# Kernel tuning notes

Measured on AMD Instinct MI355X. Metric: run time of the kernel, lower is better.

## Reference

```python
import jax, jax.numpy as jnp
import numpy as np

B, P, L, D, H = 32, 256, 64, 128, 8
DH = D // H
NP_, NL, E = B * P, B * L, B * P * L
LN_EPS = 1e-5


def setup_inputs() -> dict:
    key = jax.random.key(0)
    ks = jax.random.split(key, 32)
    def rn(i, shape, scale=0.05):
        return jax.random.normal(ks[i], shape, dtype=jnp.float32) * scale
    # uniform batch layout: graph b owns protein nodes [b*P,(b+1)*P) and ligand nodes [b*L,(b+1)*L)
    pe = (np.arange(B)[:, None] * P + np.repeat(np.arange(P), L)[None, :]).reshape(-1)
    le = (np.arange(B)[:, None] * L + np.tile(np.arange(L), P)[None, :]).reshape(-1)
    return {
        'h_protein': rn(0, (NP_, D), 1.0), 'h_ligand': rn(1, (NL, D), 1.0),
        'p_edge_idx': jnp.asarray(pe, jnp.int32), 'l_edge_idx': jnp.asarray(le, jnp.int32),
        'Wq_l': rn(2, (D, D)), 'Wk_p': rn(3, (D, D)), 'Wv_p': rn(4, (D, D)),
        'Wg_l': rn(5, (2 * D, D)), 'bg_l': jnp.zeros((D,), jnp.float32),
        'Wu_l': rn(6, (D, D)), 'bu_l': jnp.zeros((D,), jnp.float32),
        'Wq_p': rn(7, (D, D)), 'Wk_l': rn(8, (D, D)), 'Wv_l': rn(9, (D, D)),
        'Wg_p': rn(10, (2 * D, D)), 'bg_p': jnp.zeros((D,), jnp.float32),
        'Wu_p': rn(11, (D, D)), 'bu_p': jnp.zeros((D,), jnp.float32),
        'ln_p_g': jnp.ones((D,), jnp.float32), 'ln_p_b': jnp.zeros((D,), jnp.float32),
        'ln_l_g': jnp.ones((D,), jnp.float32), 'ln_l_b': jnp.zeros((D,), jnp.float32),
        'W1_p': rn(12, (D, 4 * D)), 'b1_p': jnp.zeros((4 * D,), jnp.float32),
        'W2_p': rn(13, (4 * D, D)), 'b2_p': jnp.zeros((D,), jnp.float32),
        'W1_l': rn(14, (D, 4 * D)), 'b1_l': jnp.zeros((4 * D,), jnp.float32),
        'W2_l': rn(15, (4 * D, D)), 'b2_l': jnp.zeros((D,), jnp.float32),
    }


def _layernorm(x, g, b):
    mu = jnp.mean(x, axis=-1, keepdims=True)
    var = jnp.mean(jnp.square(x - mu), axis=-1, keepdims=True)
    return (x - mu) * jax.lax.rsqrt(var + LN_EPS) * g + b


def _seg_softmax(scores, seg, n):  # scores [E,H], seg [E]
    m = jax.ops.segment_max(scores, seg, num_segments=n)
    e = jnp.exp(scores - m[seg])
    s = jax.ops.segment_sum(e, seg, num_segments=n)
    return e / s[seg]


def _side(hq, hkv, q_edge, kv_edge, nq, Wq, Wk, Wv, Wg, bg, Wu, bu):
    q = (hq @ Wq).reshape(-1, H, DH)
    k = (hkv @ Wk).reshape(-1, H, DH)
    v = (hkv @ Wv).reshape(-1, H, DH)
    scores = jnp.sum(q[q_edge] * k[kv_edge], axis=-1) / np.sqrt(DH)  # [E,H]
    att = _seg_softmax(scores, q_edge, nq)
    ctx = jax.ops.segment_sum(v[kv_edge] * att[:, :, None], q_edge, num_segments=nq)
    ctx = ctx.reshape(nq, D)
    gate = jax.nn.sigmoid(jnp.concatenate([hq, ctx], axis=1) @ Wg + bg)
    return hq + gate * (ctx @ Wu + bu)


def reference(h_protein, h_ligand, p_edge_idx, l_edge_idx,
              Wq_l, Wk_p, Wv_p, Wg_l, bg_l, Wu_l, bu_l,
              Wq_p, Wk_l, Wv_l, Wg_p, bg_p, Wu_p, bu_p,
              ln_p_g, ln_p_b, ln_l_g, ln_l_b,
              W1_p, b1_p, W2_p, b2_p, W1_l, b1_l, W2_l, b2_l):
    n_p, n_l = h_protein.shape[0], h_ligand.shape[0]
    # ligand attends to protein
    h_l_upd = _side(h_ligand, h_protein, l_edge_idx, p_edge_idx, n_l,
                    Wq_l, Wk_p, Wv_p, Wg_l, bg_l, Wu_l, bu_l)
    # protein attends to ligand
    h_p_upd = _side(h_protein, h_ligand, p_edge_idx, l_edge_idx, n_p,
                    Wq_p, Wk_l, Wv_l, Wg_p, bg_p, Wu_p, bu_p)
    # FFN blocks (dropout = identity in eval mode)
    hp = _layernorm(h_p_upd, ln_p_g, ln_p_b)
    protein_final = h_p_upd + jax.nn.relu(hp @ W1_p + b1_p) @ W2_p + b2_p
    hl = _layernorm(h_l_upd, ln_l_g, ln_l_b)
    ligand_final = h_l_upd + jax.nn.relu(hl @ W1_l + b1_l) @ W2_l + b2_l
    return (protein_final, ligand_final)
```

## Files before the change

kernel.cpp:

```cpp
#include <hip/hip_runtime.h>
#include <hip/hip_bf16.h>

typedef __bf16 bf16x8 __attribute__((ext_vector_type(8)));
typedef __bf16 bf16x4 __attribute__((ext_vector_type(4)));
typedef float  f32x4  __attribute__((ext_vector_type(4)));
typedef unsigned short u16;

#define NPROT 8192
#define NLIG  2048
#define DMODEL 128
#define NHEAD 8
#define NBATCH 32
#define PPB 256
#define LPB 64

__device__ __forceinline__ u16 f2bf(float f){
  union { float f; unsigned int u; } v; v.f = f;
  return (u16)((v.u + 0x7FFFu + ((v.u >> 16) & 1u)) >> 16);
}

__device__ __forceinline__ bf16x8 cvt8(const float* p){
  float4 a = *(const float4*)p, b = *(const float4*)(p + 4);
  bf16x8 r;
  r[0]=(__bf16)a.x; r[1]=(__bf16)a.y; r[2]=(__bf16)a.z; r[3]=(__bf16)a.w;
  r[4]=(__bf16)b.x; r[5]=(__bf16)b.y; r[6]=(__bf16)b.z; r[7]=(__bf16)b.w;
  return r;
}

struct QkvJob { const float* A; const float* Wsrc[3]; u16* outB; int blockStart; };
struct TJob { const float* src; u16* dst; int M, K, tilesX, blockStart; };
struct L1Args {
  QkvJob qjobs[2];
  int nQkv;
  int nprep;
  TJob pjobs[10];
};

__global__ __launch_bounds__(256) void l1_kernel(L1Args a){
  __shared__ u16 Wl[64][136];
  __shared__ u16 Al[64][136];
  __shared__ float tile[32][33];
  int bid = (int)blockIdx.x;
  int tid = (int)threadIdx.x;
  if (bid < a.nQkv){
    int j = (bid >= a.qjobs[1].blockStart) ? 1 : 0;
    const QkvJob jb = a.qjobs[j];
    int t = bid - jb.blockStart;
    int tn = t / 6, tm = t - tn * 6;
    {
      int midx = tm >> 1;
      int cb64 = (tm & 1) * 64;
      const float* Ws = jb.Wsrc[midx];
      int kr = tid >> 2;
      int cb = (tid & 3) * 16;
      #pragma unroll
      for (int p = 0; p < 2; ++p){
        int k = p * 64 + kr;
        const float* srcp = Ws + (size_t)k * 128 + cb64 + cb;
        float4 v0 = *(const float4*)srcp,     v1 = *(const float4*)(srcp + 4);
        float4 v2 = *(const float4*)(srcp+8), v3 = *(const float4*)(srcp + 12);
        float tmp[16] = {v0.x,v0.y,v0.z,v0.w, v1.x,v1.y,v1.z,v1.w,
                         v2.x,v2.y,v2.z,v2.w, v3.x,v3.y,v3.z,v3.w};
        #pragma unroll
        for (int i = 0; i < 16; ++i) Wl[cb + i][k] = f2bf(tmp[i]);
      }
    }
    {
      const float* Asrc = jb.A + (size_t)(tn * 64) * 128;
      #pragma unroll
      for (int p = 0; p < 8; ++p){
        int idx = p * 256 + tid;
        int r = idx >> 5, c4 = (idx & 31) * 4;
        float4 v = *(const float4*)(Asrc + (size_t)r * 128 + c4);
        Al[r][c4+0] = f2bf(v.x); Al[r][c4+1] = f2bf(v.y);
        Al[r][c4+2] = f2bf(v.z); Al[r][c4+3] = f2bf(v.w);
      }
    }
    __syncthreads();
    int w = tid >> 6, l = tid & 63;
    int rloc = (w >> 1) * 32;
    int cloc = (w & 1) * 32;
    int lr = l & 15, lk = (l >> 4) * 8;
    f32x4 a00 = {0.f,0.f,0.f,0.f}, a01 = a00, a10 = a00, a11 = a00;
    #pragma unroll
    for (int kk = 0; kk < 128; kk += 32){
      bf16x8 a0 = *(const bf16x8*)&Al[rloc + lr][kk + lk];
      bf16x8 a1 = *(const bf16x8*)&Al[rloc + 16 + lr][kk + lk];
      bf16x8 b0 = *(const bf16x8*)&Wl[cloc + lr][kk + lk];
      bf16x8 b1 = *(const bf16x8*)&Wl[cloc + 16 + lr][kk + lk];
      a00 = __builtin_amdgcn_mfma_f32_16x16x32_bf16(a0, b0, a00, 0, 0, 0);
      a01 = __builtin_amdgcn_mfma_f32_16x16x32_bf16(a0, b1, a01, 0, 0, 0);
      a10 = __builtin_amdgcn_mfma_f32_16x16x32_bf16(a1, b0, a10, 0, 0, 0);
      a11 = __builtin_amdgcn_mfma_f32_16x16x32_bf16(a1, b1, a11, 0, 0, 0);
    }
    int rbase = tn * 64 + rloc + ((l >> 4) << 2);
    f32x4 av[2][2] = {{a00, a01}, {a10, a11}};
    #pragma unroll
    for (int i = 0; i < 2; ++i)
      #pragma unroll
      for (int jj = 0; jj < 2; ++jj)
        #pragma unroll
        for (int e = 0; e < 4; ++e){
          int rr = rbase + i * 16 + e;
          int cc = tm * 64 + cloc + jj * 16 + lr;
          jb.outB[(size_t)rr * 384 + cc] = f2bf(av[i][jj][e]);
        }
  } else {
    int pb = bid - a.nQkv;
    int j = 0;
    while (j + 1 < a.nprep && pb >= a.pjobs[j + 1].blockStart) ++j;
    const TJob jb = a.pjobs[j];
    int t = pb - jb.blockStart;
    int tm = t % jb.tilesX, tk = t / jb.tilesX;
    int c = tid & 31, r0 = tid >> 5;
    #pragma unroll
    for (int p = 0; p < 4; ++p)
      tile[r0 + p * 8][c] = jb.src[(size_t)(tk * 32 + r0 + p * 8) * jb.M + tm * 32 + c];
    __syncthreads();
    {
      int c2 = tid >> 7;
      int lch = (tid >> 1) & 63;
      int eh = (tid & 1) * 4;
      int kl = (lch >> 4) * 8 + eh;
      int ml = c2 * 16 + (lch & 15);
      ushort4 o;
      o.x = f2bf(tile[kl + 0][ml]);
      o.y = f2bf(tile[kl + 1][ml]);
      o.z = f2bf(tile[kl + 2][ml]);
      o.w = f2bf(tile[kl + 3][ml]);
      size_t off = ((size_t)(tm * 2 + c2) * (jb.K >> 5) + tk) * 512 + lch * 8 + eh;
      *(ushort4*)&jb.dst[off] = o;
    }
  }
}

struct K2Args {
  const u16 *qkv_p, *qkv_l;
  const float *h_f[2];
  const u16 *WgT[2], *WgB[2], *WuT[2];
  const float *bg[2], *bu[2], *lng[2], *lnb[2];
  const u16 *W1T[2], *W2T[2];
  const float *b1[2], *b2[2];
  float* out[2];
};

struct K2B {
  float hu[32 * 132];
  union { float hstg[32 * 132]; u16 t[32 * 520]; } x;
};

__global__ __launch_bounds__(512) void k2_kernel(K2Args args){
  __shared__ __align__(16) union {
    struct { u16 vT[8 * 1152]; u16 P[8 * 2304]; } a;
    K2B b;
  } su;
  __shared__ __align__(16) u16 s_ctx[32 * 128];

  int bid = (int)blockIdx.x;
  int tid = (int)threadIdx.x;
  int w = tid >> 6, l = tid & 63, lr = l & 15, lg4 = l >> 4;
  int lk = lg4 * 8;

  int side, rowbase, batch, NC;
  if (bid < NLIG / 32){ side = 1; rowbase = bid * 32; batch = rowbase >> 6; NC = 4; }
  else { side = 0; rowbase = (bid - NLIG / 32) * 32; batch = rowbase >> 8; NC = 1; }

  const u16* qrow = (side == 0 ? args.qkv_p : args.qkv_l) + (size_t)rowbase * 384;
  const u16* orow = (side == 0 ? args.qkv_l : args.qkv_p)
                    + (size_t)(side == 0 ? batch * LPB : batch * PPB) * 384;

  bf16x8 zero8;
  #pragma unroll
  for (int i = 0; i < 8; ++i) zero8[i] = (__bf16)0.f;

  u16* vTw = su.a.vT + w * 1152;
  u16* Pw  = su.a.P  + w * 2304;
  int h = w;

  {
    bf16x8 qf[2];
    #pragma unroll
    for (int qt = 0; qt < 2; ++qt)
      qf[qt] = (l < 32) ? *(const bf16x8*)(qrow + (size_t)(qt * 16 + lr) * 384 + h * 16 + lk) : zero8;
    f32x4 Ot[2]; float mv[2], ls[2];
    #pragma unroll
    for (int qt = 0; qt < 2; ++qt){ Ot[qt] = (f32x4){0.f,0.f,0.f,0.f}; mv[qt] = -1e30f; ls[qt] = 0.f; }
    for (int c = 0; c < NC; ++c){
      {
        const u16* vs = orow + (size_t)(c * 64 + l) * 384 + 256 + h * 16;
        bf16x8 v0 = *(const bf16x8*)vs;
        bf16x8 v1 = *(const bf16x8*)(vs + 8);
        #pragma unroll
        for (int i = 0; i < 8; ++i){
          vTw[i * 72 + l]       = ((const u16*)&v0)[i];
          vTw[(i + 8) * 72 + l] = ((const u16*)&v1)[i];
        }
      }
      bf16x8 kf[4];
      #pragma unroll
      for (int kt = 0; kt < 4; ++kt)
        kf[kt] = (l < 32) ? *(const bf16x8*)(orow + (size_t)(c * 64 + kt * 16 + lr) * 384 + 128 + h * 16 + lk) : zero8;
      f32x4 sa[4][2];
      #pragma unroll
      for (int kt = 0; kt < 4; ++kt)
        #pragma unroll
        for (int qt = 0; qt < 2; ++qt)
          sa[kt][qt] = __builtin_amdgcn_mfma_f32_16x16x32_bf16(kf[kt], qf[qt], (f32x4){0.f,0.f,0.f,0.f}, 0, 0, 0);
      #pragma unroll
      for (int qt = 0; qt < 2; ++qt){
        float cm = -1e30f;
        #pragma unroll
        for (int kt = 0; kt < 4; ++kt)
          #pragma unroll
          for (int e = 0; e < 4; ++e) cm = fmaxf(cm, sa[kt][qt][e]);
        cm = fmaxf(cm, __shfl_xor(cm, 16)); cm = fmaxf(cm, __shfl_xor(cm, 32));
        float mn = fmaxf(mv[qt], cm);
        float resc = __expf((mv[qt] - mn) * 0.25f);
        mv[qt] = mn;
        float cs = 0.f;
        #pragma unroll
        for (int kt = 0; kt < 4; ++kt){
          bf16x4 pk;
          #pragma unroll
          for (int e = 0; e < 4; ++e){
            float p = __expf((sa[kt][qt][e] - mn) * 0.25f);
            cs += p; pk[e] = (__bf16)p;
          }
          *(bf16x4*)&Pw[(size_t)(qt * 16 + lr) * 72 + kt * 16 + lg4 * 4] = pk;
        }
        cs += __shfl_xor(cs, 16); cs += __shfl_xor(cs, 32);
        ls[qt] = ls[qt] * resc + cs;
        Ot[qt] = Ot[qt] * resc;
      }
      #pragma unroll
      for (int ks = 0; ks < 2; ++ks){
        bf16x8 va = *(const bf16x8*)&vTw[(size_t)lr * 72 + ks * 32 + lg4 * 8];
        #pragma unroll
        for (int qt = 0; qt < 2; ++qt){
          bf16x8 pb = *(const bf16x8*)&Pw[(size_t)(qt * 16 + lr) * 72 + ks * 32 + lg4 * 8];
          Ot[qt] = __builtin_amdgcn_mfma_f32_16x16x32_bf16(va, pb, Ot[qt], 0, 0, 0);
        }
      }
    }
    #pragma unroll
    for (int qt = 0; qt < 2; ++qt){
      float inv = 1.f / ls[qt];
      int q = qt * 16 + lr;
      int dbase = h * 16 + lg4 * 4;
      bf16x4 ov;
      #pragma unroll
      for (int e = 0; e < 4; ++e) ov[e] = (__bf16)(Ot[qt][e] * inv);
      *(bf16x4*)&s_ctx[(size_t)q * 128 + (dbase ^ ((q & 7) << 3))] = ov;
    }
  }
  __syncthreads();

  {
    const float* hsrc = args.h_f[side] + (size_t)rowbase * 128;
    #pragma unroll
    for (int p = 0; p < 2; ++p){
      int idx = p * 512 + tid;
      int r = idx >> 5, c4 = (idx & 31) * 4;
      *(float4*)&su.b.x.hstg[(size_t)r * 132 + c4] = *(const float4*)(hsrc + (size_t)r * 128 + c4);
    }
  }
  __syncthreads();

  {
    bf16x8 wg[4], wc[4], wu[4];
    {
      const u16* bgp = args.WgT[side] + (size_t)(w * 4) * 512 + l * 8;
      const u16* bcp = args.WgB[side] + (size_t)(w * 4) * 512 + l * 8;
      const u16* bup = args.WuT[side] + (size_t)(w * 4) * 512 + l * 8;
      #pragma unroll
      for (int kb = 0; kb < 4; ++kb) wg[kb] = *(const bf16x8*)(bgp + kb * 512);
      #pragma unroll
      for (int kb = 0; kb < 4; ++kb) wc[kb] = *(const bf16x8*)(bcp + kb * 512);
      #pragma unroll
      for (int kb = 0; kb < 4; ++kb) wu[kb] = *(const bf16x8*)(bup + kb * 512);
    }
    f32x4 g0 = {0.f,0.f,0.f,0.f}, g1 = g0, u0 = g0, u1 = g0;
    const float* hst = su.b.x.hstg;
    int swa = (lr & 7) << 3;
    #pragma unroll
    for (int kb = 0; kb < 4; ++kb){
      int kk = kb * 32;
      bf16x8 ah0 = cvt8(hst + (size_t)lr * 132 + kk);
      bf16x8 ah1 = cvt8(hst + (size_t)(16 + lr) * 132 + kk);
      bf16x8 ac0 = *(const bf16x8*)&s_ctx[(size_t)lr * 128 + ((kk + lk) ^ swa)];
      bf16x8 ac1 = *(const bf16x8*)&s_ctx[(size_t)(16 + lr) * 128 + ((kk + lk) ^ swa)];
      g0 = __builtin_amdgcn_mfma_f32_16x16x32_bf16(ah0, wg[kb], g0, 0, 0, 0);
      g1 = __builtin_amdgcn_mfma_f32_16x16x32_bf16(ah1, wg[kb], g1, 0, 0, 0);
      g0 = __builtin_amdgcn_mfma_f32_16x16x32_bf16(ac0, wc[kb], g0, 0, 0, 0);
      g1 = __builtin_amdgcn_mfma_f32_16x16x32_bf16(ac1, wc[kb], g1, 0, 0, 0);
      u0 = __builtin_amdgcn_mfma_f32_16x16x32_bf16(ac0, wu[kb], u0, 0, 0, 0);
      u1 = __builtin_amdgcn_mfma_f32_16x16x32_bf16(ac1, wu[kb], u1, 0, 0, 0);
    }
    int col = w * 16 + lr;
    float bgc = args.bg[side][col];
    float buc = args.bu[side][col];
    #pragma unroll
    for (int i = 0; i < 2; ++i){
      f32x4 gv4 = i ? g1 : g0;
      f32x4 uv4 = i ? u1 : u0;
      #pragma unroll
      for (int e = 0; e < 4; ++e){
        int row = i * 16 + lg4 * 4 + e;
        float gv = gv4[e] + bgc;
        float uv = uv4[e] + buc;
        float hv = hst[(size_t)row * 132 + col];
        float sg = 1.f / (1.f + __expf(-gv));
        su.b.hu[(size_t)row * 132 + col] = hv + sg * uv;
      }
    }
  }
  __syncthreads();

  {
    int r = tid >> 4;
    int sub = tid & 15;
    float x[8];
    #pragma unroll
    for (int i = 0; i < 2; ++i){
      float4 v4 = *(const float4*)&su.b.hu[(size_t)r * 132 + sub * 8 + i * 4];
      x[i*4+0] = v4.x; x[i*4+1] = v4.y; x[i*4+2] = v4.z; x[i*4+3] = v4.w;
    }
    float s = 0.f;
    #pragma unroll
    for (int i = 0; i < 8; ++i) s += x[i];
    s += __shfl_xor(s, 1); s += __shfl_xor(s, 2); s += __shfl_xor(s, 4); s += __shfl_xor(s, 8);
    float mu = s * (1.f / 128.f);
    float vv = 0.f;
    #pragma unroll
    for (int i = 0; i < 8; ++i){ float d = x[i] - mu; vv += d * d; }
    vv += __shfl_xor(vv, 1); vv += __shfl_xor(vv, 2); vv += __shfl_xor(vv, 4); vv += __shfl_xor(vv, 8);
    float rs = rsqrtf(vv * (1.f / 128.f) + 1e-5f);
    const float* lg2 = args.lng[side];
    const float* lb = args.lnb[side];
    int sw = (r & 7) << 3;
    #pragma unroll
    for (int i = 0; i < 8; ++i){
      int col = sub * 8 + i;
      s_ctx[(size_t)r * 128 + (col ^ sw)] = f2bf((x[i] - mu) * rs * lg2[col] + lb[col]);
    }
  }
  __syncthreads();

  {
    bf16x8 w1f[16];
    {
      const u16* b1p = args.W1T[side] + (size_t)(w * 16) * 512 + l * 8;
      #pragma unroll
      for (int q = 0; q < 16; ++q) w1f[q] = *(const bf16x8*)(b1p + q * 512);
    }
    f32x4 acc[2][4];
    #pragma unroll
    for (int i = 0; i < 2; ++i)
      #pragma unroll
      for (int jj = 0; jj < 4; ++jj) acc[i][jj] = (f32x4){0.f,0.f,0.f,0.f};
    int sw0 = (lr & 7) << 3;
    #pragma unroll
    for (int kb = 0; kb < 4; ++kb){
      int kk = kb * 32;
      bf16x8 a0 = *(const bf16x8*)&s_ctx[(size_t)lr * 128 + ((kk + lk) ^ sw0)];
      bf16x8 a1 = *(const bf16x8*)&s_ctx[(size_t)(16 + lr) * 128 + ((kk + lk) ^ sw0)];
      #pragma unroll
      for (int jj = 0; jj < 4; ++jj){
        acc[0][jj] = __builtin_amdgcn_mfma_f32_16x16x32_bf16(a0, w1f[jj * 4 + kb], acc[0][jj], 0, 0, 0);
        acc[1][jj] = __builtin_amdgcn_mfma_f32_16x16x32_bf16(a1, w1f[jj * 4 + kb], acc[1][jj], 0, 0, 0);
      }
    }
    const float* b1v = args.b1[side];
    u16* t_flat = su.b.x.t;
    #pragma unroll
    for (int i = 0; i < 2; ++i)
      #pragma unroll
      for (int jj = 0; jj < 4; ++jj)
        #pragma unroll
        for (int e = 0; e < 4; ++e){
          int row = i * 16 + lg4 * 4 + e;
          int col = w * 64 + jj * 16 + lr;
          float v = fmaxf(acc[i][jj][e] + b1v[col], 0.f);
          t_flat[(size_t)row * 520 + (col ^ ((row & 7) << 3))] = f2bf(v);
        }
  }
  __syncthreads();

  {
    bf16x8 w2f[16];
    {
      const u16* b2p = args.W2T[side] + (size_t)(w * 16) * 512 + l * 8;
      #pragma unroll
      for (int q = 0; q < 16; ++q) w2f[q] = *(const bf16x8*)(b2p + q * 512);
    }
    f32x4 o[2][2];
    #pragma unroll
    for (int i = 0; i < 2; ++i)
      #pragma unroll
      for (int p = 0; p < 2; ++p) o[i][p] = (f32x4){0.f,0.f,0.f,0.f};
    const u16* t_flat = su.b.x.t;
    int sw0 = (lr & 7) << 3;
    #pragma unroll
    for (int kb = 0; kb < 16; kb += 2){
      int kk = kb * 32;
      bf16x8 a0e = *(const bf16x8*)&t_flat[(size_t)lr * 520 + ((kk + lk) ^ sw0)];
      bf16x8 a1e = *(const bf16x8*)&t_flat[(size_t)(16 + lr) * 520 + ((kk + lk) ^ sw0)];
      bf16x8 a0o = *(const bf16x8*)&t_flat[(size_t)lr * 520 + ((kk + 32 + lk) ^ sw0)];
      bf16x8 a1o = *(const bf16x8*)&t_flat[(size_t)(16 + lr) * 520 + ((kk + 32 + lk) ^ sw0)];
      o[0][0] = __builtin_amdgcn_mfma_f32_16x16x32_bf16(a0e, w2f[kb],     o[0][0], 0, 0, 0);
      o[1][0] = __builtin_amdgcn_mfma_f32_16x16x32_bf16(a1e, w2f[kb],     o[1][0], 0, 0, 0);
      o[0][1] = __builtin_amdgcn_mfma_f32_16x16x32_bf16(a0o, w2f[kb + 1], o[0][1], 0, 0, 0);
      o[1][1] = __builtin_amdgcn_mfma_f32_16x16x32_bf16(a1o, w2f[kb + 1], o[1][1], 0, 0, 0);
    }
    const float* b2v = args.b2[side];
    float* outp = args.out[side];
    int col = w * 16 + lr;
    float b2c = b2v[col];
    #pragma unroll
    for (int i = 0; i < 2; ++i){
      #pragma unroll
      for (int e = 0; e < 4; ++e){
        int row = i * 16 + lg4 * 4 + e;
        float val = o[i][0][e] + o[i][1][e] + b2c + su.b.hu[(size_t)row * 132 + col];
        outp[(size_t)(rowbase + row) * 128 + col] = val;
      }
    }
  }
}

extern "C" void kernel_launch(void* const* d_in, const int* in_sizes, int n_in,
                              void* d_out, int out_size, void* d_ws, size_t ws_size,
                              hipStream_t stream) {
  (void)in_sizes; (void)n_in; (void)out_size; (void)ws_size;
  const float* h_p  = (const float*)d_in[0];
  const float* h_l  = (const float*)d_in[1];
  const float* Wq_l = (const float*)d_in[4];
  const float* Wk_p = (const float*)d_in[5];
  const float* Wv_p = (const float*)d_in[6];
  const float* Wg_l = (const float*)d_in[7];
  const float* bg_l = (const float*)d_in[8];
  const float* Wu_l = (const float*)d_in[9];
  const float* bu_l = (const float*)d_in[10];
  const float* Wq_p = (const float*)d_in[11];
  const float* Wk_l = (const float*)d_in[12];
  const float* Wv_l = (const float*)d_in[13];
  const float* Wg_p = (const float*)d_in[14];
  const float* bg_p = (const float*)d_in[15];
  const float* Wu_p = (const float*)d_in[16];
  const float* bu_p = (const float*)d_in[17];
  const float* ln_p_g = (const float*)d_in[18];
  const float* ln_p_b = (const float*)d_in[19];
  const float* ln_l_g = (const float*)d_in[20];
  const float* ln_l_b = (const float*)d_in[21];
  const float* W1_p = (const float*)d_in[22];
  const float* b1_p = (const float*)d_in[23];
  const float* W2_p = (const float*)d_in[24];
  const float* b2_p = (const float*)d_in[25];
  const float* W1_l = (const float*)d_in[26];
  const float* b1_l = (const float*)d_in[27];
  const float* W2_l = (const float*)d_in[28];
  const float* b2_l = (const float*)d_in[29];
  float* out = (float*)d_out;

  char* ws = (char*)d_ws;
  size_t off = 0;
  auto alloc = [&](size_t bytes) -> void* {
    void* p = ws + off; off += (bytes + 255) & ~(size_t)255; return p;
  };
  u16* WgT_p_T = (u16*)alloc((size_t)128 * 128 * 2);
  u16* WgB_p_T = (u16*)alloc((size_t)128 * 128 * 2);
  u16* Wu_p_T  = (u16*)alloc((size_t)128 * 128 * 2);
  u16* WgT_l_T = (u16*)alloc((size_t)128 * 128 * 2);
  u16* WgB_l_T = (u16*)alloc((size_t)128 * 128 * 2);
  u16* Wu_l_T  = (u16*)alloc((size_t)128 * 128 * 2);
  u16* W1_p_T  = (u16*)alloc((size_t)512 * 128 * 2);
  u16* W1_l_T  = (u16*)alloc((size_t)512 * 128 * 2);
  u16* W2_p_T  = (u16*)alloc((size_t)128 * 512 * 2);
  u16* W2_l_T  = (u16*)alloc((size_t)128 * 512 * 2);
  u16* qkv_p   = (u16*)alloc((size_t)NPROT * 384 * 2);
  u16* qkv_l   = (u16*)alloc((size_t)NLIG  * 384 * 2);

  {
    L1Args a;
    a.qjobs[0] = { h_p, {Wq_p, Wk_p, Wv_p}, qkv_p, 0 };
    a.qjobs[1] = { h_l, {Wq_l, Wk_l, Wv_l}, qkv_l, (NPROT / 64) * 6 };
    a.nQkv = (NPROT / 64) * 6 + (NLIG / 64) * 6;
    int pbs = 0;
    int pi = 0;
    auto addT = [&](const float* s, u16* d, int K, int M){
      a.pjobs[pi].src = s; a.pjobs[pi].dst = d; a.pjobs[pi].M = M; a.pjobs[pi].K = K;
      a.pjobs[pi].tilesX = M / 32; a.pjobs[pi].blockStart = pbs;
      pbs += (K / 32) * (M / 32); ++pi;
    };
    addT(Wg_l,             WgT_l_T, 128, 128);
    addT(Wg_l + 128 * 128, WgB_l_T, 128, 128);
    addT(Wu_l,             Wu_l_T,  128, 128);
    addT(Wg_p,             WgT_p_T, 128, 128);
    addT(Wg_p + 128 * 128, WgB_p_T, 128, 128);
    addT(Wu_p,             Wu_p_T,  128, 128);
    addT(W1_p, W1_p_T, 128, 512);
    addT(W2_p, W2_p_T, 512, 128);
    addT(W1_l, W1_l_T, 128, 512);
    addT(W2_l, W2_l_T, 512, 128);
    a.nprep = pi;
    l1_kernel<<<dim3(a.nQkv + pbs), dim3(256), 0, stream>>>(a);
  }

  {
    K2Args k;
    k.qkv_p = qkv_p; k.qkv_l = qkv_l;
    k.h_f[0] = h_p; k.h_f[1] = h_l;
    k.WgT[0] = WgT_p_T; k.WgT[1] = WgT_l_T;
    k.WgB[0] = WgB_p_T; k.WgB[1] = WgB_l_T;
    k.WuT[0] = Wu_p_T;  k.WuT[1] = Wu_l_T;
    k.bg[0] = bg_p; k.bg[1] = bg_l;
    k.bu[0] = bu_p; k.bu[1] = bu_l;
    k.lng[0] = ln_p_g; k.lng[1] = ln_l_g;
    k.lnb[0] = ln_p_b; k.lnb[1] = ln_l_b;
    k.W1T[0] = W1_p_T; k.W1T[1] = W1_l_T;
    k.W2T[0] = W2_p_T; k.W2T[1] = W2_l_T;
    k.b1[0] = b1_p; k.b1[1] = b1_l;
    k.b2[0] = b2_p; k.b2[1] = b2_l;
    k.out[0] = out; k.out[1] = out + (size_t)NPROT * DMODEL;
    k2_kernel<<<dim3(NLIG / 32 + NPROT / 32), dim3(512), 0, stream>>>(k);
  }
}
```

Measured before the change: 40.48 us.

## Store QKV in head-major layout with LDS-staged coalesced writes

The QKV projection output moves from a row-major [N,384] layout to a head-major [3][8][N][16] layout. Results are staged through shared memory so each thread writes two 16-byte vectors instead of scattered 2-byte stores. The attention kernel's Q/K/V loads are rewritten to read contiguous 32-byte head slices. This adds two barriers and LDS traffic in the projection kernel, and requires both kernels to agree on the new layout.

Result: faster. 39.68 us, median of 3 (-2.0%).

```diff
diff --git a/kernel.cpp b/kernel.cpp
--- a/kernel.cpp
+++ b/kernel.cpp
@@ -27,7 +27,7 @@
   return r;
 }
 
-struct QkvJob { const float* A; const float* Wsrc[3]; u16* outB; int blockStart; };
+struct QkvJob { const float* A; const float* Wsrc[3]; u16* outB; int N; int blockStart; };
 struct TJob { const float* src; u16* dst; int M, K, tilesX, blockStart; };
 struct L1Args {
   QkvJob qjobs[2];
@@ -93,18 +93,30 @@
       a10 = __builtin_amdgcn_mfma_f32_16x16x32_bf16(a1, b0, a10, 0, 0, 0);
       a11 = __builtin_amdgcn_mfma_f32_16x16x32_bf16(a1, b1, a11, 0, 0, 0);
     }
-    int rbase = tn * 64 + rloc + ((l >> 4) << 2);
-    f32x4 av[2][2] = {{a00, a01}, {a10, a11}};
-    #pragma unroll
-    for (int i = 0; i < 2; ++i)
-      #pragma unroll
-      for (int jj = 0; jj < 2; ++jj)
-        #pragma unroll
-        for (int e = 0; e < 4; ++e){
-          int rr = rbase + i * 16 + e;
-          int cc = tm * 64 + cloc + jj * 16 + lr;
-          jb.outB[(size_t)rr * 384 + cc] = f2bf(av[i][jj][e]);
-        }
+    __syncthreads();
+    {
+      f32x4 av[2][2] = {{a00, a01}, {a10, a11}};
+      int lg4 = l >> 4;
+      #pragma unroll
+      for (int i = 0; i < 2; ++i)
+        #pragma unroll
+        for (int jj = 0; jj < 2; ++jj)
+          #pragma unroll
+          for (int e = 0; e < 4; ++e)
+            Al[rloc + i * 16 + lg4 * 4 + e][cloc + jj * 16 + lr] = f2bf(av[i][jj][e]);
+    }
+    __syncthreads();
+    {
+      int row = tid >> 2;
+      int hseg = tid & 3;
+      int m = tm >> 1;
+      int h = (tm & 1) * 4 + hseg;
+      const u16* srcl = &Al[row][hseg * 16];
+      u16* dst = jb.outB + ((size_t)m * NHEAD + h) * (size_t)jb.N * 16
+                         + (size_t)(tn * 64 + row) * 16;
+      *(bf16x8*)dst = *(const bf16x8*)srcl;
+      *(bf16x8*)(dst + 8) = *(const bf16x8*)(srcl + 8);
+    }
   } else {
     int pb = bid - a.nQkv;
     int j = 0;
@@ -165,9 +177,13 @@
   if (bid < NLIG / 32){ side = 1; rowbase = bid * 32; batch = rowbase >> 6; NC = 4; }
   else { side = 0; rowbase = (bid - NLIG / 32) * 32; batch = rowbase >> 8; NC = 1; }
 
-  const u16* qrow = (side == 0 ? args.qkv_p : args.qkv_l) + (size_t)rowbase * 384;
-  const u16* orow = (side == 0 ? args.qkv_l : args.qkv_p)
-                    + (size_t)(side == 0 ? batch * LPB : batch * PPB) * 384;
+  int NRs = side == 0 ? NPROT : NLIG;
+  int NRo = side == 0 ? NLIG : NPROT;
+  int orowoff = side == 0 ? batch * LPB : batch * PPB;
+  const u16* qbase = (side == 0 ? args.qkv_p : args.qkv_l);
+  const u16* obase = (side == 0 ? args.qkv_l : args.qkv_p);
+  const u16* kbase = obase + (size_t)NHEAD * NRo * 16;
+  const u16* vbase = obase + (size_t)2 * NHEAD * NRo * 16;
 
   bf16x8 zero8;
   #pragma unroll
@@ -181,13 +197,15 @@
     bf16x8 qf[2];
     #pragma unroll
     for (int qt = 0; qt < 2; ++qt)
-      qf[qt] = (l < 32) ? *(const bf16x8*)(qrow + (size_t)(qt * 16 + lr) * 384 + h * 16 + lk) : zero8;
+      qf[qt] = (l < 32)
+        ? *(const bf16x8*)(qbase + ((size_t)h * NRs + rowbase + qt * 16 + lr) * 16 + lk)
+        : zero8;
     f32x4 Ot[2]; float mv[2], ls[2];
     #pragma unroll
     for (int qt = 0; qt < 2; ++qt){ Ot[qt] = (f32x4){0.f,0.f,0.f,0.f}; mv[qt] = -1e30f; ls[qt] = 0.f; }
     for (int c = 0; c < NC; ++c){
       {
-        const u16* vs = orow + (size_t)(c * 64 + l) * 384 + 256 + h * 16;
+        const u16* vs = vbase + ((size_t)h * NRo + orowoff + c * 64 + l) * 16;
         bf16x8 v0 = *(const bf16x8*)vs;
         bf16x8 v1 = *(const bf16x8*)(vs + 8);
         #pragma unroll
@@ -199,7 +217,9 @@
       bf16x8 kf[4];
       #pragma unroll
       for (int kt = 0; kt < 4; ++kt)
-        kf[kt] = (l < 32) ? *(const bf16x8*)(orow + (size_t)(c * 64 + kt * 16 + lr) * 384 + 128 + h * 16 + lk) : zero8;
+        kf[kt] = (l < 32)
+          ? *(const bf16x8*)(kbase + ((size_t)h * NRo + orowoff + c * 64 + kt * 16 + lr) * 16 + lk)
+          : zero8;
       f32x4 sa[4][2];
       #pragma unroll
       for (int kt = 0; kt < 4; ++kt)
@@ -482,8 +502,8 @@
 
   {
     L1Args a;
-    a.qjobs[0] = { h_p, {Wq_p, Wk_p, Wv_p}, qkv_p, 0 };
-    a.qjobs[1] = { h_l, {Wq_l, Wk_l, Wv_l}, qkv_l, (NPROT / 64) * 6 };
+    a.qjobs[0] = { h_p, {Wq_p, Wk_p, Wv_p}, qkv_p, NPROT, 0 };
+    a.qjobs[1] = { h_l, {Wq_l, Wk_l, Wv_l}, qkv_l, NLIG, (NPROT / 64) * 6 };
     a.nQkv = (NPROT / 64) * 6 + (NLIG / 64) * 6;
     int pbs = 0;
     int pi = 0;
```
